# Kernel optimization log

Hardware: AMD Instinct MI355X
Metric: run time of the kernel (lower is better)

## Reference

```python
import jax, jax.numpy as jnp
import numpy as np

# ViT-Small config
L, D, H, HD = 12, 384, 6, 64
P, IMG, NCLS = 16, 224, 1000
NPATCH = (IMG // P) ** 2  # 196
GAMMA, MIN_TOKENS, EPS = 0.5, 16, 1e-6
SCALE = HD ** -0.5


def _ln(x, w, b, eps=1e-6):
    mu = jnp.mean(x, axis=-1, keepdims=True)
    var = jnp.var(x, axis=-1, keepdims=True)
    return (x - mu) * jax.lax.rsqrt(var + eps) * w + b


def _qkv_split(xn, w, b):
    # xn: [B, Nt, D] -> q,k,v each [B, H, Nt, HD]
    B, Nt, _ = xn.shape
    qkv = (xn @ w.T + b).reshape(B, Nt, 3, H, HD).transpose(2, 0, 3, 1, 4)
    return qkv[0], qkv[1], qkv[2]


def _vit_forward(x, patch_w, patch_b, cls_token, pos_embed,
                 ln1_w, ln1_b, qkv_w, qkv_b, proj_w, proj_b,
                 ln2_w, ln2_b, fc1_w, fc1_b, fc2_w, fc2_b,
                 norm_w, norm_b, head_w, head_b, keep_schedule=None):
    B = x.shape[0]
    # patch embed: conv stride 16 -> [B, D, 14, 14] -> [B, 196, D]
    xp = jax.lax.conv_general_dilated(x, patch_w, (P, P), 'VALID',
                                      dimension_numbers=('NCHW', 'OIHW', 'NCHW'))
    xp = xp.reshape(B, D, NPATCH).transpose(0, 2, 1) + patch_b
    cls = jnp.broadcast_to(cls_token, (B, 1, D))
    xt = jnp.concatenate([cls, xp], axis=1) + pos_embed  # [B, 197, D]

    N = NPATCH
    prev_mass = jnp.asarray(1.0, jnp.float32)
    schedule = []
    for l in range(L):
        if keep_schedule is not None:
            keep_idx = keep_schedule[l]
        elif N > MIN_TOKENS:
            # CLS-only attention importance scoring (cheap pass)
            xn = _ln(xt, ln1_w[l], ln1_b[l])
            q, k, v = _qkv_split(xn, qkv_w[l], qkv_b[l])
            a_cls = jax.nn.softmax(jnp.einsum('bhqd,bhkd->bhqk', q[:, :, :1], k) * SCALE, axis=-1)[:, :, 0, :]  # [B,H,Nt]
            vnorm = jnp.linalg.norm(v, axis=-1)  # [B,H,Nt]
            imp = (a_cls * vnorm).mean(axis=1)   # [B,Nt]
            imp_p = imp[:, 1:]                   # patch importance
            mass = jnp.mean(imp_p.sum(-1) / (imp.sum(-1) + EPS))
            keep_ratio = float(jnp.clip(GAMMA * mass / (prev_mass + EPS), 0.0, 1.0))
            N_next = max(MIN_TOKENS, int(N * keep_ratio))
            if N_next < N:
                scores = imp_p.mean(0)  # shared keep set across batch (index_select semantics)
                top = jax.lax.top_k(scores, N_next)[1]
                keep_idx = jnp.concatenate([jnp.zeros((1,), jnp.int32),
                                            jnp.sort(top).astype(jnp.int32) + 1])
            else:
                keep_idx = None
            prev_mass = mass
        else:
            keep_idx = None
        schedule.append(keep_idx)
        if keep_idx is not None:
            xt = jnp.take(xt, keep_idx, axis=1)
            N = int(keep_idx.shape[0]) - 1

        # full transformer block on surviving tokens
        Nt = xt.shape[1]
        xn = _ln(xt, ln1_w[l], ln1_b[l])
        q, k, v = _qkv_split(xn, qkv_w[l], qkv_b[l])
        a = jax.nn.softmax(jnp.einsum('bhqd,bhkd->bhqk', q, k) * SCALE, axis=-1)
        o = jnp.einsum('bhqk,bhkd->bhqd', a, v).transpose(0, 2, 1, 3).reshape(B, Nt, D)
        xt = xt + o @ proj_w[l].T + proj_b[l]
        h = _ln(xt, ln2_w[l], ln2_b[l])
        h = jax.nn.gelu(h @ fc1_w[l].T + fc1_b[l], approximate=False)
        xt = xt + h @ fc2_w[l].T + fc2_b[l]

    xt = _ln(xt, norm_w, norm_b)
    logits = xt[:, 0] @ head_w.T + head_b
    return logits, schedule


def setup_inputs() -> dict:
    key = jax.random.key(0)
    ks = jax.random.split(key, 10)
    rn = lambda k, s, sc=0.02: jax.random.normal(k, s, jnp.float32) * sc
    return {
        'x': jax.random.normal(ks[0], (64, 3, IMG, IMG), jnp.float32),
        'patch_w': rn(ks[1], (D, 3, P, P)),
        'patch_b': jnp.zeros((D,), jnp.float32),
        'cls_token': rn(ks[2], (1, 1, D)),
        'pos_embed': rn(ks[3], (1, NPATCH + 1, D)),
        'ln1_w': jnp.ones((L, D), jnp.float32), 'ln1_b': jnp.zeros((L, D), jnp.float32),
        'qkv_w': rn(ks[4], (L, 3 * D, D)), 'qkv_b': jnp.zeros((L, 3 * D), jnp.float32),
        'proj_w': rn(ks[5], (L, D, D)), 'proj_b': jnp.zeros((L, D), jnp.float32),
        'ln2_w': jnp.ones((L, D), jnp.float32), 'ln2_b': jnp.zeros((L, D), jnp.float32),
        'fc1_w': rn(ks[6], (L, 4 * D, D)), 'fc1_b': jnp.zeros((L, 4 * D), jnp.float32),
        'fc2_w': rn(ks[7], (L, D, 4 * D)), 'fc2_b': jnp.zeros((L, D), jnp.float32),
        'norm_w': jnp.ones((D,), jnp.float32), 'norm_b': jnp.zeros((D,), jnp.float32),
        'head_w': rn(ks[8], (NCLS, D)), 'head_b': jnp.zeros((NCLS,), jnp.float32),
    }


def reference(x, patch_w, patch_b, cls_token, pos_embed, ln1_w, ln1_b, qkv_w, qkv_b,
              proj_w, proj_b, ln2_w, ln2_b, fc1_w, fc1_b, fc2_w, fc2_b,
              norm_w, norm_b, head_w, head_b):
    logits, _ = _vit_forward(x, patch_w, patch_b, cls_token, pos_embed, ln1_w, ln1_b,
                             qkv_w, qkv_b, proj_w, proj_b, ln2_w, ln2_b,
                             fc1_w, fc1_b, fc2_w, fc2_b, norm_w, norm_b, head_w, head_b)
    return logits
```

## Files before the change

kernel.cpp:

```cpp
#include <hip/hip_runtime.h>
#include <hip/hip_bf16.h>

static constexpr int kL = 12;
static constexpr int kD = 384;
static constexpr int kH = 6;
static constexpr int kB = 64;
static constexpr int kNP = 196;
static constexpr int kBAND = 197;
static constexpr int kNCLS = 1000;
static constexpr float kSCALE = 0.125f;
static constexpr float kEPS = 1e-6f;
static constexpr size_t kWQ = (size_t)kB * kH * kBAND * 64;

typedef __attribute__((ext_vector_type(8))) short short8;
typedef __attribute__((ext_vector_type(4))) float f32x4;

__device__ __forceinline__ float gelu_f(float x) {
    return 0.5f * x * (1.0f + erff(x * 0.70710678118654752440f));
}
__device__ __forceinline__ unsigned short f2bf(float x) {
    __hip_bfloat16 h = __float2bfloat16(x);
    return *(unsigned short*)&h;
}
__device__ __forceinline__ float bf2f(unsigned short u) {
    __hip_bfloat16 h = *(__hip_bfloat16*)&u;
    return __bfloat162float(h);
}

__global__ __launch_bounds__(384) void k_init(int* si, float* sf,
                                              const float* __restrict__ cls,
                                              const float* __restrict__ pos,
                                              float* __restrict__ xtA,
                                              float2* __restrict__ pstats) {
    int b = blockIdx.x, c = threadIdx.x;
    float v = cls[c] + pos[c];
    xtA[(size_t)b * kBAND * kD + c] = v;
    __shared__ float r1[384], r2[384];
    r1[c] = v; r2[c] = v * v;
    __syncthreads();
    if (c < 128) { r1[c] += r1[c + 128] + r1[c + 256]; r2[c] += r2[c + 128] + r2[c + 256]; }
    __syncthreads();
    for (int st = 64; st; st >>= 1) {
        if (c < st) { r1[c] += r1[c + st]; r2[c] += r2[c + st]; }
        __syncthreads();
    }
    if (c == 0) {
        pstats[(size_t)(b * kBAND) * 8 + 0] = make_float2(r1[0], r2[0]);
#pragma unroll
        for (int nn = 1; nn < 6; ++nn) pstats[(size_t)(b * kBAND) * 8 + nn] = make_float2(0.f, 0.f);
        if (b == 0) { si[0] = kBAND; sf[0] = 1.0f; }
    }
}

__global__ __launch_bounds__(256) void k_cvtall(
    const float* __restrict__ s0, const float* __restrict__ s1, const float* __restrict__ s2,
    const float* __restrict__ s3, const float* __restrict__ s4,
    __hip_bfloat16* __restrict__ d0, __hip_bfloat16* __restrict__ d1, __hip_bfloat16* __restrict__ d2,
    __hip_bfloat16* __restrict__ d3, __hip_bfloat16* __restrict__ d4) {
    const int c0 = 73728, c1 = 1400832, c2 = 1843200, c3 = 3612672, c4 = 5382144;
    int stride = gridDim.x * 256;
    for (int i = blockIdx.x * 256 + threadIdx.x; i < c4; i += stride) {
        const float* src; __hip_bfloat16* dst; int off;
        if (i < c0)      { src = s0; dst = d0; off = i; }
        else if (i < c1) { src = s1; dst = d1; off = i - c0; }
        else if (i < c2) { src = s2; dst = d2; off = i - c1; }
        else if (i < c3) { src = s3; dst = d3; off = i - c2; }
        else             { src = s4; dst = d4; off = i - c3; }
        float4 v = ((const float4*)src)[off];
        dst[4 * off + 0] = __float2bfloat16(v.x);
        dst[4 * off + 1] = __float2bfloat16(v.y);
        dst[4 * off + 2] = __float2bfloat16(v.z);
        dst[4 * off + 3] = __float2bfloat16(v.w);
    }
}

__global__ __launch_bounds__(256) void k_im2col(const float* __restrict__ x, __hip_bfloat16* __restrict__ A) {
    int pt = blockIdx.x;
    int b = pt / kNP, t = pt - b * kNP;
    int py = t / 14, px = t - py * 14;
    const float* xb = x + (size_t)b * 3 * 224 * 224;
    __hip_bfloat16* arow = A + (size_t)pt * 768;
    for (int k = threadIdx.x; k < 768; k += 256) {
        int c = k >> 8;
        int r = k & 255;
        int ky = r >> 4, kx = r & 15;
        arow[k] = __float2bfloat16(xb[((size_t)c * 224 + py * 16 + ky) * 224 + px * 16 + kx]);
    }
}

template<int OUT_BF16, int ACT_GELU, int MODE, int LNA, int STATS>
__global__ __launch_bounds__(256) void k_mgemm(
    const void* __restrict__ Av, int lda,
    const unsigned short* __restrict__ W, int K,
    const float* __restrict__ bias,
    void* __restrict__ Cv, int ldc,
    const float* __restrict__ R,
    const int* __restrict__ keepR,
    const float* __restrict__ lnw, const float* __restrict__ lnb,
    int rT, int nT, int band,
    const int* __restrict__ NtPtr, int ntConst,
    const float2* __restrict__ pstatsIn, float2* __restrict__ pstatsOut)
{
    __shared__ __align__(16) unsigned char pool[18432];
    unsigned short (*As)[72] = (unsigned short (*)[72])pool;
    unsigned short (*Ws)[72] = (unsigned short (*)[72])(pool + 9216);
    float (*Cs)[66] = (float (*)[66])pool;
    unsigned short (*Cu)[76] = (unsigned short (*)[76])pool;
    __shared__ float mus[64], rss[64];

    int Nt = NtPtr ? NtPtr[0] : ntConst;
    unsigned int rowsTotal = (unsigned int)kB * (unsigned int)Nt;

    int L = blockIdx.x;
    int xcd = L & 7;
    int m = L >> 3;
    int n = m % nT;
    int r = (m / nT) * 8 + xcd;
    if (r >= rT) return;
    unsigned int r0 = (unsigned int)r * 64;
    int n0 = n * 64;
    if (r0 >= rowsTotal) return;

    int tid = threadIdx.x;
    int srow = tid >> 3;
    int scol = (tid & 7) << 3;

    unsigned int rv0 = r0 + srow, rv1 = r0 + srow + 32;
    bool v0 = rv0 < rowsTotal, v1 = rv1 < rowsTotal;
    const unsigned short* ah0 = nullptr; const unsigned short* ah1 = nullptr;
    const float* af0 = nullptr; const float* af1 = nullptr;
    if (v0) {
        unsigned int bb = rv0 / (unsigned int)Nt, tt = rv0 - bb * Nt;
        size_t prow = (size_t)bb * band + tt;
        if (LNA) af0 = (const float*)Av + prow * lda;
        else     ah0 = (const unsigned short*)Av + prow * lda;
    }
    if (v1) {
        unsigned int bb = rv1 / (unsigned int)Nt, tt = rv1 - bb * Nt;
        size_t prow = (size_t)bb * band + tt;
        if (LNA) af1 = (const float*)Av + prow * lda;
        else     ah1 = (const unsigned short*)Av + prow * lda;
    }
    const unsigned short* wp0 = W + (size_t)(n0 + srow) * K;
    const unsigned short* wp1 = W + (size_t)(n0 + srow + 32) * K;

    float mu0 = 0.f, rs0 = 0.f, mu1 = 0.f, rs1 = 0.f;
    if (LNA) {
        if (tid < 64) {
            unsigned int rv = r0 + tid;
            float mu = 0.f, rsd = 0.f;
            if (rv < rowsTotal) {
                unsigned int bb = rv / (unsigned int)Nt, tt = rv - bb * Nt;
                const float2* ps = pstatsIn + ((size_t)bb * band + tt) * 8;
                float s1 = 0.f, s2 = 0.f;
#pragma unroll
                for (int nn = 0; nn < 6; ++nn) { float2 p = ps[nn]; s1 += p.x; s2 += p.y; }
                mu = s1 * (1.f / 384.f);
                float var = fmaxf(s2 * (1.f / 384.f) - mu * mu, 0.f);
                rsd = rsqrtf(var + kEPS);
            }
            mus[tid] = mu; rss[tid] = rsd;
        }
        __syncthreads();
        mu0 = mus[srow]; rs0 = rss[srow];
        mu1 = mus[srow + 32]; rs1 = rss[srow + 32];
    }

    int wave = tid >> 6, lane = tid & 63;
    int wr32 = ((wave >> 1) & 1) * 32, wc32 = (wave & 1) * 32;
    int l15 = lane & 15, l4 = lane >> 4;

    f32x4 acc00 = {}, acc01 = {}, acc10 = {}, acc11 = {};

    for (int k0 = 0; k0 < K; k0 += 64) {
        uint4 zero = make_uint4(0, 0, 0, 0);
        uint4 a0 = zero, a1 = zero;
        uint4 w0 = *(const uint4*)(wp0 + k0 + scol);
        uint4 w1 = *(const uint4*)(wp1 + k0 + scol);
        if (LNA) {
            float4 lw0 = *(const float4*)(lnw + k0 + scol);
            float4 lw1 = *(const float4*)(lnw + k0 + scol + 4);
            float4 lb0 = *(const float4*)(lnb + k0 + scol);
            float4 lb1 = *(const float4*)(lnb + k0 + scol + 4);
            if (v0) {
                float4 x0 = *(const float4*)(af0 + k0 + scol);
                float4 x1 = *(const float4*)(af0 + k0 + scol + 4);
                unsigned short p[8];
                p[0] = f2bf((x0.x - mu0) * rs0 * lw0.x + lb0.x);
                p[1] = f2bf((x0.y - mu0) * rs0 * lw0.y + lb0.y);
                p[2] = f2bf((x0.z - mu0) * rs0 * lw0.z + lb0.z);
                p[3] = f2bf((x0.w - mu0) * rs0 * lw0.w + lb0.w);
                p[4] = f2bf((x1.x - mu0) * rs0 * lw1.x + lb1.x);
                p[5] = f2bf((x1.y - mu0) * rs0 * lw1.y + lb1.y);
                p[6] = f2bf((x1.z - mu0) * rs0 * lw1.z + lb1.z);
                p[7] = f2bf((x1.w - mu0) * rs0 * lw1.w + lb1.w);
                a0 = *(uint4*)p;
            }
            if (v1) {
                float4 x0 = *(const float4*)(af1 + k0 + scol);
                float4 x1 = *(const float4*)(af1 + k0 + scol + 4);
                unsigned short p[8];
                p[0] = f2bf((x0.x - mu1) * rs1 * lw0.x + lb0.x);
                p[1] = f2bf((x0.y - mu1) * rs1 * lw0.y + lb0.y);
                p[2] = f2bf((x0.z - mu1) * rs1 * lw0.z + lb0.z);
                p[3] = f2bf((x0.w - mu1) * rs1 * lw0.w + lb0.w);
                p[4] = f2bf((x1.x - mu1) * rs1 * lw1.x + lb1.x);
                p[5] = f2bf((x1.y - mu1) * rs1 * lw1.y + lb1.y);
                p[6] = f2bf((x1.z - mu1) * rs1 * lw1.z + lb1.z);
                p[7] = f2bf((x1.w - mu1) * rs1 * lw1.w + lb1.w);
                a1 = *(uint4*)p;
            }
        } else {
            a0 = v0 ? *(const uint4*)(ah0 + k0 + scol) : zero;
            a1 = v1 ? *(const uint4*)(ah1 + k0 + scol) : zero;
        }
        __syncthreads();
        *(uint4*)&As[srow][scol] = a0;
        *(uint4*)&As[srow + 32][scol] = a1;
        *(uint4*)&Ws[srow][scol] = w0;
        *(uint4*)&Ws[srow + 32][scol] = w1;
        __syncthreads();
#pragma unroll
        for (int ks = 0; ks < 2; ++ks) {
            short8 af_0 = *(const short8*)&As[wr32 + l15][ks * 32 + l4 * 8];
            short8 af_1 = *(const short8*)&As[wr32 + 16 + l15][ks * 32 + l4 * 8];
            short8 bf_0 = *(const short8*)&Ws[wc32 + l15][ks * 32 + l4 * 8];
            short8 bf_1 = *(const short8*)&Ws[wc32 + 16 + l15][ks * 32 + l4 * 8];
            acc00 = __builtin_amdgcn_mfma_f32_16x16x32_bf16(af_0, bf_0, acc00, 0, 0, 0);
            acc01 = __builtin_amdgcn_mfma_f32_16x16x32_bf16(af_0, bf_1, acc01, 0, 0, 0);
            acc10 = __builtin_amdgcn_mfma_f32_16x16x32_bf16(af_1, bf_0, acc10, 0, 0, 0);
            acc11 = __builtin_amdgcn_mfma_f32_16x16x32_bf16(af_1, bf_1, acc11, 0, 0, 0);
        }
    }

    __syncthreads();
    f32x4 accs[2][2] = { { acc00, acc01 }, { acc10, acc11 } };
#pragma unroll
    for (int fi = 0; fi < 2; ++fi) {
        int lrow = wr32 + fi * 16 + l4 * 4;
        unsigned int rvb = r0 + lrow;
#pragma unroll
        for (int fj = 0; fj < 2; ++fj) {
            int lcol = wc32 + fj * 16 + l15;
            float bv = bias ? bias[n0 + lcol] : 0.f;
#pragma unroll
            for (int rr = 0; rr < 4; ++rr) {
                unsigned int rv = rvb + rr;
                float v = accs[fi][fj][rr] + bv;
                if (ACT_GELU) v = gelu_f(v);
                if (MODE == 2) {
                    if (rv < rowsTotal) {
                        unsigned int bb = rv / (unsigned int)Nt;
                        unsigned int tt = rv - bb * (unsigned int)Nt;
                        v += R[(size_t)(tt + 1) * kD + n0 + lcol];
                    }
                } else if (R && rv < rowsTotal) {
                    unsigned int bb = rv / (unsigned int)Nt;
                    unsigned int tt = rv - bb * (unsigned int)Nt;
                    size_t rrow = keepR ? ((size_t)bb * band + keepR[tt]) : ((size_t)bb * band + tt);
                    v += R[rrow * ldc + n0 + lcol];
                }
                if (OUT_BF16) Cu[lrow + rr][lcol] = f2bf(v);
                else          Cs[lrow + rr][lcol] = v;
            }
        }
    }
    __syncthreads();

    if (OUT_BF16) {
#pragma unroll
        for (int i = 0; i < 2; ++i) {
            int id = tid + (i << 8);
            int row = id >> 3, c2 = id & 7;
            unsigned int rv = r0 + row;
            if (rv < rowsTotal) {
                unsigned int bb = rv / (unsigned int)Nt;
                unsigned int tt = rv - bb * (unsigned int)Nt;
                uint4 val = *(const uint4*)&Cu[row][c2 << 3];
                if (MODE == 1) {
                    int which = n0 >= 768 ? 2 : (n0 >= 384 ? 1 : 0);
                    int hh = (n0 - which * 384) >> 6;
                    *(uint4*)((__hip_bfloat16*)Cv + (size_t)which * kWQ +
                              (((size_t)bb * kH + hh) * kBAND + tt) * 64 + (c2 << 3)) = val;
                } else {
                    size_t prow = (size_t)bb * band + tt;
                    *(uint4*)((__hip_bfloat16*)Cv + prow * ldc + n0 + (c2 << 3)) = val;
                }
            }
        }
    } else {
#pragma unroll
        for (int i = 0; i < 4; ++i) {
            int id = tid + (i << 8);
            int row = id >> 4, c4 = id & 15;
            unsigned int rv = r0 + row;
            if (rv < rowsTotal) {
                unsigned int bb = rv / (unsigned int)Nt;
                unsigned int tt = rv - bb * (unsigned int)Nt;
                float4 val = *(const float4*)&Cs[row][c4 << 2];
                if (MODE == 2) {
                    *(float4*)((float*)Cv + ((size_t)bb * kBAND + tt + 1) * ldc + n0 + (c4 << 2)) = val;
                } else {
                    *(float4*)((float*)Cv + ((size_t)bb * band + tt) * ldc + n0 + (c4 << 2)) = val;
                }
                if (STATS) {
                    float s1 = (val.x + val.y) + (val.z + val.w);
                    float s2 = (val.x * val.x + val.y * val.y) + (val.z * val.z + val.w * val.w);
#pragma unroll
                    for (int off = 1; off < 16; off <<= 1) {
                        s1 += __shfl_xor(s1, off, 64);
                        s2 += __shfl_xor(s2, off, 64);
                    }
                    if (c4 == 0) {
                        size_t sridx = (MODE == 2) ? ((size_t)bb * kBAND + tt + 1)
                                                   : ((size_t)bb * band + tt);
                        pstatsOut[sridx * 8 + n] = make_float2(s1, s2);
                    }
                }
            }
        }
    }
}

__global__ __launch_bounds__(256) void k_decA(const __hip_bfloat16* __restrict__ qsplit,
                                              float* __restrict__ imph, float* __restrict__ sabh,
                                              const int* __restrict__ si) {
    int Nt = si[0];
    if (Nt - 1 <= 16) return;
    int tid = threadIdx.x, w = tid >> 6, lane = tid & 63;
    int bh = blockIdx.x;
    __shared__ float qs[64];
    __shared__ float sdot[224], svn[224];
    __shared__ float red[256];
    const __hip_bfloat16* qp = qsplit + (size_t)bh * kBAND * 64;
    const __hip_bfloat16* kp = qsplit + kWQ + (size_t)bh * kBAND * 64;
    const __hip_bfloat16* vp = qsplit + 2 * kWQ + (size_t)bh * kBAND * 64;
    if (tid < 64) qs[tid] = __bfloat162float(qp[tid]);
    __syncthreads();
    float qv = qs[lane];
    for (int j = w; j < Nt; j += 8) {
        int j2 = j + 4;
        bool has2 = j2 < Nt;
        float k1 = __bfloat162float(kp[(size_t)j * 64 + lane]);
        float v1 = __bfloat162float(vp[(size_t)j * 64 + lane]);
        float k2 = has2 ? __bfloat162float(kp[(size_t)j2 * 64 + lane]) : 0.f;
        float v2 = has2 ? __bfloat162float(vp[(size_t)j2 * 64 + lane]) : 0.f;
        float p1 = qv * k1, n1 = v1 * v1;
        float p2 = qv * k2, n2 = v2 * v2;
#pragma unroll
        for (int off = 1; off < 64; off <<= 1) {
            p1 += __shfl_xor(p1, off, 64); n1 += __shfl_xor(n1, off, 64);
            p2 += __shfl_xor(p2, off, 64); n2 += __shfl_xor(n2, off, 64);
        }
        if (lane == 0) {
            sdot[j] = p1 * kSCALE; svn[j] = sqrtf(n1);
            if (has2) { sdot[j2] = p2 * kSCALE; svn[j2] = sqrtf(n2); }
        }
    }
    __syncthreads();
    float s = (tid < Nt) ? sdot[tid] : -INFINITY;
    red[tid] = s; __syncthreads();
    for (int st = 128; st; st >>= 1) { if (tid < st) red[tid] = fmaxf(red[tid], red[tid + st]); __syncthreads(); }
    float mmax = red[0]; __syncthreads();
    float e = (tid < Nt) ? expf(s - mmax) : 0.f;
    red[tid] = e; __syncthreads();
    for (int st = 128; st; st >>= 1) { if (tid < st) red[tid] += red[tid + st]; __syncthreads(); }
    float inv = 1.f / red[0];
    float val = (tid < Nt) ? e * inv * svn[tid] : 0.f;
    if (tid < Nt) imph[(size_t)bh * kBAND + tid] = val;
    __syncthreads();
    red[tid] = val; __syncthreads();
    for (int st = 128; st; st >>= 1) { if (tid < st) red[tid] += red[tid + st]; __syncthreads(); }
    if (tid == 0) { sabh[2 * bh] = red[0]; sabh[2 * bh + 1] = val; }
}

__global__ __launch_bounds__(256) void k_decB(int* __restrict__ si, float* __restrict__ sf,
                                              const float* __restrict__ imph,
                                              const float* __restrict__ sabh,
                                              int* __restrict__ keep) {
    int Nt = si[0];
    int tid = threadIdx.x;
    if (Nt - 1 <= 16) {
        for (int j = tid; j < Nt; j += 256) keep[j] = j;
        return;
    }
    int N = Nt - 1;
    __shared__ float red[256];
    float v = 0.f;
    if (tid < kB) {
        float sa = 0.f, i0 = 0.f;
#pragma unroll
        for (int hh = 0; hh < kH; ++hh) {
            sa += sabh[2 * (tid * kH + hh)];
            i0 += sabh[2 * (tid * kH + hh) + 1];
        }
        sa *= (1.f / 6.f); i0 *= (1.f / 6.f);
        v = (sa - i0) / (sa + kEPS);
    }
    red[tid] = v; __syncthreads();
    for (int st = 128; st; st >>= 1) { if (tid < st) red[tid] += red[tid + st]; __syncthreads(); }
    float mass = red[0] * (1.f / 64.f);
    float prev = sf[0];
    float ratio = 0.5f * mass / (prev + kEPS);
    ratio = fminf(fmaxf(ratio, 0.f), 1.f);
    int N_next = (int)((double)N * (double)ratio);
    if (N_next < 16) N_next = 16;
    if (tid == 0) sf[0] = mass;
    __syncthreads();
    if (N_next >= N) {
        for (int j = tid; j < Nt; j += 256) keep[j] = j;
        return;
    }
    __shared__ float sc[200];
    __shared__ int flag[200];
    if (tid < N) {
        float a0 = 0.f, a1 = 0.f, a2 = 0.f, a3 = 0.f;
        const float* p = imph + tid + 1;
#pragma unroll 4
        for (int q = 0; q < kB * kH; q += 4) {
            a0 += p[(size_t)(q + 0) * kBAND];
            a1 += p[(size_t)(q + 1) * kBAND];
            a2 += p[(size_t)(q + 2) * kBAND];
            a3 += p[(size_t)(q + 3) * kBAND];
        }
        sc[tid] = (a0 + a1) + (a2 + a3);
    }
    __syncthreads();
    if (tid < N) {
        float s2 = sc[tid];
        int rank = 0;
        for (int i = 0; i < N; ++i) {
            float o2 = sc[i];
            rank += (o2 > s2) || (o2 == s2 && i < tid);
        }
        flag[tid] = (rank < N_next) ? 1 : 0;
    }
    __syncthreads();
    if (tid == 0) {
        keep[0] = 0;
        int pos = 1;
        for (int j = 0; j < N; ++j) if (flag[j]) keep[pos++] = j + 1;
        si[0] = N_next + 1;
    }
}

__global__ __launch_bounds__(256) void k_attn2(const __hip_bfloat16* __restrict__ qsplit,
                                               __hip_bfloat16* __restrict__ o,
                                               const int* __restrict__ si,
                                               const int* __restrict__ keep) {
    __shared__ __align__(16) unsigned short Kb[224][72];
    __shared__ __align__(16) unsigned short Vt[64][228];
    __shared__ __align__(16) unsigned short Pb[4][16][228];
    int Nt = si[0];
    int bh = blockIdx.x;
    int b = bh / kH, h = bh - b * kH;
    int tid = threadIdx.x, w = tid >> 6, lane = tid & 63;
    int l15 = lane & 15, l4 = lane >> 4;
    int nJT = (Nt + 15) >> 4;
    int nKT = (Nt + 31) >> 5;
    int NTP = nKT << 5;

    const unsigned short* qb = (const unsigned short*)qsplit + (size_t)bh * kBAND * 64;
    const unsigned short* kb = (const unsigned short*)qsplit + kWQ + (size_t)bh * kBAND * 64;
    const unsigned short* vb = (const unsigned short*)qsplit + 2 * kWQ + (size_t)bh * kBAND * 64;

    {
        int rr = tid >> 3;
        int c8 = (tid & 7) << 3;
        for (int r = rr; r < NTP; r += 32) {
            uint4 kv = make_uint4(0, 0, 0, 0), vv = make_uint4(0, 0, 0, 0);
            if (r < Nt) {
                int old = keep[r];
                kv = *(const uint4*)(kb + ((size_t)old << 6) + c8);
                vv = *(const uint4*)(vb + ((size_t)old << 6) + c8);
            }
            *(uint4*)&Kb[r][c8] = kv;
            const unsigned short* vs = (const unsigned short*)&vv;
#pragma unroll
            for (int e = 0; e < 8; ++e) Vt[c8 + e][r] = vs[e];
        }
    }
    __syncthreads();

    for (int strip = w; strip < nJT; strip += 4) {
        int tq = (strip << 4) + l15;
        int told = (tq < Nt) ? keep[tq] : 0;
        const unsigned short* qrow = qb + ((size_t)told << 6) + (l4 << 3);
        short8 qf0 = *(const short8*)(qrow);
        short8 qf1 = *(const short8*)(qrow + 32);

        f32x4 sv[13];
#pragma unroll
        for (int jt = 0; jt < 13; ++jt) {
            if (jt < nJT) {
                const unsigned short* kr = &Kb[(jt << 4) + l15][l4 << 3];
                short8 kf0 = *(const short8*)(kr);
                short8 kf1 = *(const short8*)(kr + 32);
                f32x4 a = {};
                a = __builtin_amdgcn_mfma_f32_16x16x32_bf16(qf0, kf0, a, 0, 0, 0);
                a = __builtin_amdgcn_mfma_f32_16x16x32_bf16(qf1, kf1, a, 0, 0, 0);
                sv[jt] = a;
            }
        }
        float mx[4] = { -INFINITY, -INFINITY, -INFINITY, -INFINITY };
#pragma unroll
        for (int jt = 0; jt < 13; ++jt) if (jt < nJT) {
            bool ok = ((jt << 4) + l15) < Nt;
#pragma unroll
            for (int r = 0; r < 4; ++r) {
                float s = ok ? sv[jt][r] * kSCALE : -INFINITY;
                sv[jt][r] = s;
                mx[r] = fmaxf(mx[r], s);
            }
        }
#pragma unroll
        for (int r = 0; r < 4; ++r) {
            mx[r] = fmaxf(mx[r], __shfl_xor(mx[r], 1, 64));
            mx[r] = fmaxf(mx[r], __shfl_xor(mx[r], 2, 64));
            mx[r] = fmaxf(mx[r], __shfl_xor(mx[r], 4, 64));
            mx[r] = fmaxf(mx[r], __shfl_xor(mx[r], 8, 64));
        }
        float sm[4] = { 0.f, 0.f, 0.f, 0.f };
#pragma unroll
        for (int jt = 0; jt < 13; ++jt) if (jt < nJT) {
#pragma unroll
            for (int r = 0; r < 4; ++r) {
                float p = expf(sv[jt][r] - mx[r]);
                sv[jt][r] = p;
                sm[r] += p;
            }
        }
#pragma unroll
        for (int r = 0; r < 4; ++r) {
            sm[r] += __shfl_xor(sm[r], 1, 64);
            sm[r] += __shfl_xor(sm[r], 2, 64);
            sm[r] += __shfl_xor(sm[r], 4, 64);
            sm[r] += __shfl_xor(sm[r], 8, 64);
            sm[r] = 1.f / sm[r];
        }
#pragma unroll
        for (int jt = 0; jt < 13; ++jt) if (jt < nJT) {
#pragma unroll
            for (int r = 0; r < 4; ++r)
                Pb[w][(l4 << 2) + r][(jt << 4) + l15] = f2bf(sv[jt][r] * sm[r]);
        }
        for (int c = (nJT << 4) + lane; c < NTP; c += 64) {
#pragma unroll
            for (int rr2 = 0; rr2 < 16; ++rr2) Pb[w][rr2][c] = 0;
        }
        asm volatile("s_waitcnt lgkmcnt(0)" ::: "memory");
        __builtin_amdgcn_sched_barrier(0);

        f32x4 oacc[4] = { {}, {}, {}, {} };
#pragma unroll
        for (int kt = 0; kt < 7; ++kt) if (kt < nKT) {
            short8 pf = *(const short8*)&Pb[w][l15][(kt << 5) + (l4 << 3)];
#pragma unroll
            for (int dt = 0; dt < 4; ++dt) {
                short8 vf = *(const short8*)&Vt[(dt << 4) + l15][(kt << 5) + (l4 << 3)];
                oacc[dt] = __builtin_amdgcn_mfma_f32_16x16x32_bf16(pf, vf, oacc[dt], 0, 0, 0);
            }
        }
#pragma unroll
        for (int dt = 0; dt < 4; ++dt) {
#pragma unroll
            for (int r = 0; r < 4; ++r) {
                int tqo = (strip << 4) + (l4 << 2) + r;
                if (tqo < Nt)
                    o[((size_t)b * kBAND + tqo) * kD + h * 64 + (dt << 4) + l15] =
                        __float2bfloat16(oacc[dt][r]);
            }
        }
    }
}

__global__ __launch_bounds__(256) void k_head(const float* __restrict__ X,
                                              const float* __restrict__ nw, const float* __restrict__ nb,
                                              const float* __restrict__ hw, const float* __restrict__ hb,
                                              float* __restrict__ out) {
    int b = blockIdx.x >> 2;
    int tid = threadIdx.x;
    __shared__ float xs[384];
    __shared__ float red[256];
    const float* row = X + (size_t)b * kBAND * kD;
    float s1 = 0.f, s2 = 0.f;
    for (int c = tid; c < 384; c += 256) { float v = row[c]; xs[c] = v; s1 += v; s2 += v * v; }
    red[tid] = s1; __syncthreads();
    for (int st = 128; st; st >>= 1) { if (tid < st) red[tid] += red[tid + st]; __syncthreads(); }
    float sum = red[0]; __syncthreads();
    red[tid] = s2; __syncthreads();
    for (int st = 128; st; st >>= 1) { if (tid < st) red[tid] += red[tid + st]; __syncthreads(); }
    float sq = red[0];
    float mu = sum * (1.f / 384.f);
    float var = fmaxf(sq * (1.f / 384.f) - mu * mu, 0.f);
    float rs = rsqrtf(var + kEPS);
    __syncthreads();
    for (int c = tid; c < 384; c += 256) xs[c] = (xs[c] - mu) * rs * nw[c] + nb[c];
    __syncthreads();
    int n = ((blockIdx.x & 3) << 8) + tid;
    if (n >= kNCLS) return;
    const float* wrow = hw + (size_t)n * kD;
    float acc = 0.f;
#pragma unroll 8
    for (int d = 0; d < kD; d += 4) {
        float4 w4 = *(const float4*)(wrow + d);
        acc += xs[d] * w4.x + xs[d + 1] * w4.y + xs[d + 2] * w4.z + xs[d + 3] * w4.w;
    }
    out[(size_t)b * kNCLS + n] = acc + hb[n];
}

extern "C" void kernel_launch(void* const* d_in, const int* in_sizes, int n_in,
                              void* d_out, int out_size, void* d_ws, size_t ws_size,
                              hipStream_t stream) {
    const float* x       = (const float*)d_in[0];
    const float* patch_w = (const float*)d_in[1];
    const float* patch_b = (const float*)d_in[2];
    const float* cls_tok = (const float*)d_in[3];
    const float* pos     = (const float*)d_in[4];
    const float* ln1w    = (const float*)d_in[5];
    const float* ln1b    = (const float*)d_in[6];
    const float* qkvw    = (const float*)d_in[7];
    const float* qkvb    = (const float*)d_in[8];
    const float* projw   = (const float*)d_in[9];
    const float* projb   = (const float*)d_in[10];
    const float* ln2w    = (const float*)d_in[11];
    const float* ln2b    = (const float*)d_in[12];
    const float* fc1w    = (const float*)d_in[13];
    const float* fc1b    = (const float*)d_in[14];
    const float* fc2w    = (const float*)d_in[15];
    const float* fc2b    = (const float*)d_in[16];
    const float* normw   = (const float*)d_in[17];
    const float* normb   = (const float*)d_in[18];
    const float* headw   = (const float*)d_in[19];
    const float* headb   = (const float*)d_in[20];
    float* out = (float*)d_out;

    char* ws = (char*)d_ws;
    const size_t MB = 1024ull * 1024ull;
    int*   si   = (int*)ws;
    float* sf   = (float*)(ws + 64);
    int*   keep = (int*)(ws + 256);
    float* sabh = (float*)(ws + 4096);
    float* imph = (float*)(ws + 16384);
    float* xtA  = (float*)(ws + 1 * MB);
    float* xtB  = (float*)(ws + 21 * MB);
    __hip_bfloat16* obuf = (__hip_bfloat16*)(ws + 41 * MB);
    __hip_bfloat16* Aim    = (__hip_bfloat16*)(ws + 51 * MB);
    __hip_bfloat16* qsplit = (__hip_bfloat16*)(ws + 51 * MB);
    __hip_bfloat16* hbuf   = (__hip_bfloat16*)(ws + 51 * MB);
    __hip_bfloat16* wpat = (__hip_bfloat16*)(ws + 110 * MB);
    __hip_bfloat16* wqkv = (__hip_bfloat16*)(ws + 111 * MB);
    __hip_bfloat16* wprj = (__hip_bfloat16*)(ws + 122 * MB);
    __hip_bfloat16* wfc1 = (__hip_bfloat16*)(ws + 126 * MB);
    __hip_bfloat16* wfc2 = (__hip_bfloat16*)(ws + 141 * MB);
    float2* pstats = (float2*)(ws + 156 * MB);

    k_init<<<64, 384, 0, stream>>>(si, sf, cls_tok, pos, xtA, pstats);
    k_cvtall<<<2048, 256, 0, stream>>>(patch_w, qkvw, projw, fc1w, fc2w,
                                       wpat, wqkv, wprj, wfc1, wfc2);

    k_im2col<<<kB * kNP, 256, 0, stream>>>(x, Aim);
    k_mgemm<0, 0, 2, 0, 1><<<8 * 6 * 25, 256, 0, stream>>>(
        (const void*)Aim, 768, (const unsigned short*)wpat, 768,
        patch_b, xtA, kD, pos, (const int*)nullptr,
        (const float*)nullptr, (const float*)nullptr,
        196, 6, 196, (const int*)nullptr, 196,
        (const float2*)nullptr, pstats);

    float* cur = xtA; float* oth = xtB;
    for (int l = 0; l < kL; ++l) {
        const float* l1w = ln1w + l * kD;  const float* l1b = ln1b + l * kD;
        const __hip_bfloat16* qw = wqkv + (size_t)l * 1152 * kD;
        const float* qb = qkvb + l * 1152;
        const __hip_bfloat16* pw = wprj + (size_t)l * kD * kD;
        const float* pb = projb + l * kD;
        const float* l2w = ln2w + l * kD;  const float* l2b = ln2b + l * kD;
        const __hip_bfloat16* f1w = wfc1 + (size_t)l * 1536 * kD;
        const float* f1b = fc1b + l * 1536;
        const __hip_bfloat16* f2w = wfc2 + (size_t)l * kD * 1536;
        const float* f2b = fc2b + l * kD;

        k_mgemm<1, 0, 1, 1, 0><<<8 * 18 * 25, 256, 0, stream>>>(
            (const void*)cur, kD, (const unsigned short*)qw, kD,
            qb, qsplit, 1152, (const float*)nullptr, (const int*)nullptr,
            l1w, l1b, 197, 18, kBAND, si, 0,
            (const float2*)pstats, (float2*)nullptr);
        k_decA<<<kB * kH, 256, 0, stream>>>(qsplit, imph, sabh, si);
        k_decB<<<1, 256, 0, stream>>>(si, sf, imph, sabh, keep);
        k_attn2<<<kB * kH, 256, 0, stream>>>(qsplit, obuf, si, keep);
        k_mgemm<0, 0, 0, 0, 1><<<8 * 6 * 25, 256, 0, stream>>>(
            (const void*)obuf, kD, (const unsigned short*)pw, kD,
            pb, oth, kD, cur, keep,
            (const float*)nullptr, (const float*)nullptr,
            197, 6, kBAND, si, 0,
            (const float2*)nullptr, pstats);
        { float* tmp = cur; cur = oth; oth = tmp; }
        k_mgemm<1, 1, 0, 1, 0><<<8 * 24 * 25, 256, 0, stream>>>(
            (const void*)cur, kD, (const unsigned short*)f1w, kD,
            f1b, hbuf, 1536, (const float*)nullptr, (const int*)nullptr,
            l2w, l2b, 197, 24, kBAND, si, 0,
            (const float2*)pstats, (float2*)nullptr);
        k_mgemm<0, 0, 0, 0, 1><<<8 * 6 * 25, 256, 0, stream>>>(
            (const void*)hbuf, 1536, (const unsigned short*)f2w, 1536,
            f2b, cur, kD, cur, (const int*)nullptr,
            (const float*)nullptr, (const float*)nullptr,
            197, 6, kBAND, si, 0,
            (const float2*)nullptr, pstats);
    }

    k_head<<<kB * 4, 256, 0, stream>>>(cur, normw, normb, headw, headb, out);
}
```

Before: 1.251 ms.

## Enlarge GEMM tiles to 128x128 and transpose importance buffer for coalesced reduction

The MFMA GEMM kernel moves from 64x64 to 128x128 output tiles, with each wave computing a 4x4 grid of 16x16 fragments. The epilogue is staged in two halves through enlarged shared memory, and all launch grids are resized to match. Separately, the per-head importance array is stored token-major so the single-block keep-selection kernel can reduce it with coalesced float4 loads split across four segments. The larger tiles raise data reuse per block but use more registers and shared memory, and they give fewer blocks, which may lower occupancy and wave count as the token count shrinks.

```diff
diff --git a/kernel.cpp b/kernel.cpp
--- a/kernel.cpp
+++ b/kernel.cpp
@@ -11,6 +11,7 @@
 static constexpr float kSCALE = 0.125f;
 static constexpr float kEPS = 1e-6f;
 static constexpr size_t kWQ = (size_t)kB * kH * kBAND * 64;
+static constexpr int kBH = kB * kH;
 
 typedef __attribute__((ext_vector_type(8))) short short8;
 typedef __attribute__((ext_vector_type(4))) float f32x4;
@@ -21,10 +22,6 @@
 __device__ __forceinline__ unsigned short f2bf(float x) {
     __hip_bfloat16 h = __float2bfloat16(x);
     return *(unsigned short*)&h;
-}
-__device__ __forceinline__ float bf2f(unsigned short u) {
-    __hip_bfloat16 h = *(__hip_bfloat16*)&u;
-    return __bfloat162float(h);
 }
 
 __global__ __launch_bounds__(384) void k_init(int* si, float* sf,
@@ -101,12 +98,12 @@
     const int* __restrict__ NtPtr, int ntConst,
     const float2* __restrict__ pstatsIn, float2* __restrict__ pstatsOut)
 {
-    __shared__ __align__(16) unsigned char pool[18432];
+    __shared__ __align__(16) unsigned char pool[36928];
     unsigned short (*As)[72] = (unsigned short (*)[72])pool;
-    unsigned short (*Ws)[72] = (unsigned short (*)[72])(pool + 9216);
-    float (*Cs)[66] = (float (*)[66])pool;
-    unsigned short (*Cu)[76] = (unsigned short (*)[76])pool;
-    __shared__ float mus[64], rss[64];
+    unsigned short (*Ws)[72] = (unsigned short (*)[72])(pool + 18432);
+    float (*Cs)[136] = (float (*)[136])pool;
+    unsigned short (*Cu)[136] = (unsigned short (*)[136])pool;
+    __shared__ float mus[128], rss[128];
 
     int Nt = NtPtr ? NtPtr[0] : ntConst;
     unsigned int rowsTotal = (unsigned int)kB * (unsigned int)Nt;
@@ -117,208 +114,201 @@
     int n = m % nT;
     int r = (m / nT) * 8 + xcd;
     if (r >= rT) return;
-    unsigned int r0 = (unsigned int)r * 64;
-    int n0 = n * 64;
+    unsigned int r0 = (unsigned int)r * 128;
+    int n0 = n * 128;
     if (r0 >= rowsTotal) return;
 
     int tid = threadIdx.x;
-    int srow = tid >> 3;
-    int scol = (tid & 7) << 3;
-
-    unsigned int rv0 = r0 + srow, rv1 = r0 + srow + 32;
-    bool v0 = rv0 < rowsTotal, v1 = rv1 < rowsTotal;
-    const unsigned short* ah0 = nullptr; const unsigned short* ah1 = nullptr;
-    const float* af0 = nullptr; const float* af1 = nullptr;
-    if (v0) {
-        unsigned int bb = rv0 / (unsigned int)Nt, tt = rv0 - bb * Nt;
+    int srow = tid >> 1;
+    int scol = (tid & 1) << 5;
+
+    unsigned int rvs = r0 + srow;
+    bool vA = rvs < rowsTotal;
+    const unsigned short* ah = nullptr; const float* af = nullptr;
+    if (vA) {
+        unsigned int bb = rvs / (unsigned int)Nt, tt = rvs - bb * Nt;
         size_t prow = (size_t)bb * band + tt;
-        if (LNA) af0 = (const float*)Av + prow * lda;
-        else     ah0 = (const unsigned short*)Av + prow * lda;
-    }
-    if (v1) {
-        unsigned int bb = rv1 / (unsigned int)Nt, tt = rv1 - bb * Nt;
-        size_t prow = (size_t)bb * band + tt;
-        if (LNA) af1 = (const float*)Av + prow * lda;
-        else     ah1 = (const unsigned short*)Av + prow * lda;
-    }
-    const unsigned short* wp0 = W + (size_t)(n0 + srow) * K;
-    const unsigned short* wp1 = W + (size_t)(n0 + srow + 32) * K;
-
-    float mu0 = 0.f, rs0 = 0.f, mu1 = 0.f, rs1 = 0.f;
+        if (LNA) af = (const float*)Av + prow * lda;
+        else     ah = (const unsigned short*)Av + prow * lda;
+    }
+    const unsigned short* wp = W + (size_t)(n0 + srow) * K;
+
+    float mu = 0.f, rsd = 0.f;
     if (LNA) {
-        if (tid < 64) {
+        if (tid < 128) {
             unsigned int rv = r0 + tid;
-            float mu = 0.f, rsd = 0.f;
+            float m_ = 0.f, rr_ = 0.f;
             if (rv < rowsTotal) {
                 unsigned int bb = rv / (unsigned int)Nt, tt = rv - bb * Nt;
                 const float2* ps = pstatsIn + ((size_t)bb * band + tt) * 8;
                 float s1 = 0.f, s2 = 0.f;
 #pragma unroll
                 for (int nn = 0; nn < 6; ++nn) { float2 p = ps[nn]; s1 += p.x; s2 += p.y; }
-                mu = s1 * (1.f / 384.f);
-                float var = fmaxf(s2 * (1.f / 384.f) - mu * mu, 0.f);
-                rsd = rsqrtf(var + kEPS);
-            }
-            mus[tid] = mu; rss[tid] = rsd;
+                m_ = s1 * (1.f / 384.f);
+                float var = fmaxf(s2 * (1.f / 384.f) - m_ * m_, 0.f);
+                rr_ = rsqrtf(var + kEPS);
+            }
+            mus[tid] = m_; rss[tid] = rr_;
         }
         __syncthreads();
-        mu0 = mus[srow]; rs0 = rss[srow];
-        mu1 = mus[srow + 32]; rs1 = rss[srow + 32];
+        mu = mus[srow]; rsd = rss[srow];
     }
 
     int wave = tid >> 6, lane = tid & 63;
-    int wr32 = ((wave >> 1) & 1) * 32, wc32 = (wave & 1) * 32;
+    int wr = (wave >> 1) << 6;
+    int wc = (wave & 1) << 6;
     int l15 = lane & 15, l4 = lane >> 4;
 
-    f32x4 acc00 = {}, acc01 = {}, acc10 = {}, acc11 = {};
+    f32x4 acc[4][4];
+#pragma unroll
+    for (int i = 0; i < 4; ++i)
+#pragma unroll
+        for (int j = 0; j < 4; ++j) acc[i][j] = (f32x4){};
 
     for (int k0 = 0; k0 < K; k0 += 64) {
-        uint4 zero = make_uint4(0, 0, 0, 0);
-        uint4 a0 = zero, a1 = zero;
-        uint4 w0 = *(const uint4*)(wp0 + k0 + scol);
-        uint4 w1 = *(const uint4*)(wp1 + k0 + scol);
-        if (LNA) {
-            float4 lw0 = *(const float4*)(lnw + k0 + scol);
-            float4 lw1 = *(const float4*)(lnw + k0 + scol + 4);
-            float4 lb0 = *(const float4*)(lnb + k0 + scol);
-            float4 lb1 = *(const float4*)(lnb + k0 + scol + 4);
-            if (v0) {
-                float4 x0 = *(const float4*)(af0 + k0 + scol);
-                float4 x1 = *(const float4*)(af0 + k0 + scol + 4);
-                unsigned short p[8];
-                p[0] = f2bf((x0.x - mu0) * rs0 * lw0.x + lb0.x);
-                p[1] = f2bf((x0.y - mu0) * rs0 * lw0.y + lb0.y);
-                p[2] = f2bf((x0.z - mu0) * rs0 * lw0.z + lb0.z);
-                p[3] = f2bf((x0.w - mu0) * rs0 * lw0.w + lb0.w);
-                p[4] = f2bf((x1.x - mu0) * rs0 * lw1.x + lb1.x);
-                p[5] = f2bf((x1.y - mu0) * rs0 * lw1.y + lb1.y);
-                p[6] = f2bf((x1.z - mu0) * rs0 * lw1.z + lb1.z);
-                p[7] = f2bf((x1.w - mu0) * rs0 * lw1.w + lb1.w);
-                a0 = *(uint4*)p;
-            }
-            if (v1) {
-                float4 x0 = *(const float4*)(af1 + k0 + scol);
-                float4 x1 = *(const float4*)(af1 + k0 + scol + 4);
-                unsigned short p[8];
-                p[0] = f2bf((x0.x - mu1) * rs1 * lw0.x + lb0.x);
-                p[1] = f2bf((x0.y - mu1) * rs1 * lw0.y + lb0.y);
-                p[2] = f2bf((x0.z - mu1) * rs1 * lw0.z + lb0.z);
-                p[3] = f2bf((x0.w - mu1) * rs1 * lw0.w + lb0.w);
-                p[4] = f2bf((x1.x - mu1) * rs1 * lw1.x + lb1.x);
-                p[5] = f2bf((x1.y - mu1) * rs1 * lw1.y + lb1.y);
-                p[6] = f2bf((x1.z - mu1) * rs1 * lw1.z + lb1.z);
-                p[7] = f2bf((x1.w - mu1) * rs1 * lw1.w + lb1.w);
-                a1 = *(uint4*)p;
-            }
-        } else {
-            a0 = v0 ? *(const uint4*)(ah0 + k0 + scol) : zero;
-            a1 = v1 ? *(const uint4*)(ah1 + k0 + scol) : zero;
+        uint4 a[4], wv[4];
+#pragma unroll
+        for (int e = 0; e < 4; ++e) {
+            wv[e] = *(const uint4*)(wp + k0 + scol + (e << 3));
+            if (LNA) {
+                if (vA) {
+                    const float* ap = af + k0 + scol + (e << 3);
+                    float4 x0 = *(const float4*)(ap);
+                    float4 x1 = *(const float4*)(ap + 4);
+                    float4 lw0 = *(const float4*)(lnw + k0 + scol + (e << 3));
+                    float4 lw1 = *(const float4*)(lnw + k0 + scol + (e << 3) + 4);
+                    float4 lb0 = *(const float4*)(lnb + k0 + scol + (e << 3));
+                    float4 lb1 = *(const float4*)(lnb + k0 + scol + (e << 3) + 4);
+                    unsigned short p[8];
+                    p[0] = f2bf((x0.x - mu) * rsd * lw0.x + lb0.x);
+                    p[1] = f2bf((x0.y - mu) * rsd * lw0.y + lb0.y);
+                    p[2] = f2bf((x0.z - mu) * rsd * lw0.z + lb0.z);
+                    p[3] = f2bf((x0.w - mu) * rsd * lw0.w + lb0.w);
+                    p[4] = f2bf((x1.x - mu) * rsd * lw1.x + lb1.x);
+                    p[5] = f2bf((x1.y - mu) * rsd * lw1.y + lb1.y);
+                    p[6] = f2bf((x1.z - mu) * rsd * lw1.z + lb1.z);
+                    p[7] = f2bf((x1.w - mu) * rsd * lw1.w + lb1.w);
+                    a[e] = *(uint4*)p;
+                } else a[e] = make_uint4(0, 0, 0, 0);
+            } else {
+                a[e] = vA ? *(const uint4*)(ah + k0 + scol + (e << 3)) : make_uint4(0, 0, 0, 0);
+            }
         }
         __syncthreads();
-        *(uint4*)&As[srow][scol] = a0;
-        *(uint4*)&As[srow + 32][scol] = a1;
-        *(uint4*)&Ws[srow][scol] = w0;
-        *(uint4*)&Ws[srow + 32][scol] = w1;
+#pragma unroll
+        for (int e = 0; e < 4; ++e) {
+            *(uint4*)&As[srow][scol + (e << 3)] = a[e];
+            *(uint4*)&Ws[srow][scol + (e << 3)] = wv[e];
+        }
         __syncthreads();
 #pragma unroll
         for (int ks = 0; ks < 2; ++ks) {
-            short8 af_0 = *(const short8*)&As[wr32 + l15][ks * 32 + l4 * 8];
-            short8 af_1 = *(const short8*)&As[wr32 + 16 + l15][ks * 32 + l4 * 8];
-            short8 bf_0 = *(const short8*)&Ws[wc32 + l15][ks * 32 + l4 * 8];
-            short8 bf_1 = *(const short8*)&Ws[wc32 + 16 + l15][ks * 32 + l4 * 8];
-            acc00 = __builtin_amdgcn_mfma_f32_16x16x32_bf16(af_0, bf_0, acc00, 0, 0, 0);
-            acc01 = __builtin_amdgcn_mfma_f32_16x16x32_bf16(af_0, bf_1, acc01, 0, 0, 0);
-            acc10 = __builtin_amdgcn_mfma_f32_16x16x32_bf16(af_1, bf_0, acc10, 0, 0, 0);
-            acc11 = __builtin_amdgcn_mfma_f32_16x16x32_bf16(af_1, bf_1, acc11, 0, 0, 0);
-        }
-    }
-
-    __syncthreads();
-    f32x4 accs[2][2] = { { acc00, acc01 }, { acc10, acc11 } };
-#pragma unroll
-    for (int fi = 0; fi < 2; ++fi) {
-        int lrow = wr32 + fi * 16 + l4 * 4;
-        unsigned int rvb = r0 + lrow;
-#pragma unroll
-        for (int fj = 0; fj < 2; ++fj) {
-            int lcol = wc32 + fj * 16 + l15;
-            float bv = bias ? bias[n0 + lcol] : 0.f;
-#pragma unroll
-            for (int rr = 0; rr < 4; ++rr) {
-                unsigned int rv = rvb + rr;
-                float v = accs[fi][fj][rr] + bv;
-                if (ACT_GELU) v = gelu_f(v);
-                if (MODE == 2) {
-                    if (rv < rowsTotal) {
-                        unsigned int bb = rv / (unsigned int)Nt;
-                        unsigned int tt = rv - bb * (unsigned int)Nt;
-                        v += R[(size_t)(tt + 1) * kD + n0 + lcol];
+            short8 afr[4], bfr[4];
+#pragma unroll
+            for (int i = 0; i < 4; ++i)
+                afr[i] = *(const short8*)&As[wr + (i << 4) + l15][(ks << 5) + (l4 << 3)];
+#pragma unroll
+            for (int j = 0; j < 4; ++j)
+                bfr[j] = *(const short8*)&Ws[wc + (j << 4) + l15][(ks << 5) + (l4 << 3)];
+#pragma unroll
+            for (int i = 0; i < 4; ++i)
+#pragma unroll
+                for (int j = 0; j < 4; ++j)
+                    acc[i][j] = __builtin_amdgcn_mfma_f32_16x16x32_bf16(afr[i], bfr[j], acc[i][j], 0, 0, 0);
+        }
+    }
+
+    __syncthreads();
+#pragma unroll
+    for (int half = 0; half < 2; ++half) {
+        if ((wave >> 1) == half) {
+#pragma unroll
+            for (int i = 0; i < 4; ++i) {
+                int lrow = (i << 4) + (l4 << 2);
+                unsigned int rvb = r0 + (half << 6) + lrow;
+#pragma unroll
+                for (int j = 0; j < 4; ++j) {
+                    int lcol = wc + (j << 4) + l15;
+                    float bv = bias ? bias[n0 + lcol] : 0.f;
+#pragma unroll
+                    for (int rr = 0; rr < 4; ++rr) {
+                        unsigned int rv = rvb + rr;
+                        float v = acc[i][j][rr] + bv;
+                        if (ACT_GELU) v = gelu_f(v);
+                        if (MODE == 2) {
+                            if (rv < rowsTotal) {
+                                unsigned int bb = rv / (unsigned int)Nt;
+                                unsigned int tt = rv - bb * (unsigned int)Nt;
+                                v += R[(size_t)(tt + 1) * kD + n0 + lcol];
+                            }
+                        } else if (R && rv < rowsTotal) {
+                            unsigned int bb = rv / (unsigned int)Nt;
+                            unsigned int tt = rv - bb * (unsigned int)Nt;
+                            size_t rrow = keepR ? ((size_t)bb * band + keepR[tt]) : ((size_t)bb * band + tt);
+                            v += R[rrow * ldc + n0 + lcol];
+                        }
+                        if (OUT_BF16) Cu[lrow + rr][lcol] = f2bf(v);
+                        else          Cs[lrow + rr][lcol] = v;
                     }
-                } else if (R && rv < rowsTotal) {
+                }
+            }
+        }
+        __syncthreads();
+        if (OUT_BF16) {
+#pragma unroll
+            for (int i2 = 0; i2 < 4; ++i2) {
+                int id = tid + (i2 << 8);
+                int row = id >> 4, c2 = id & 15;
+                unsigned int rv = r0 + (half << 6) + row;
+                if (rv < rowsTotal) {
                     unsigned int bb = rv / (unsigned int)Nt;
                     unsigned int tt = rv - bb * (unsigned int)Nt;
-                    size_t rrow = keepR ? ((size_t)bb * band + keepR[tt]) : ((size_t)bb * band + tt);
-                    v += R[rrow * ldc + n0 + lcol];
-                }
-                if (OUT_BF16) Cu[lrow + rr][lcol] = f2bf(v);
-                else          Cs[lrow + rr][lcol] = v;
-            }
-        }
-    }
-    __syncthreads();
-
-    if (OUT_BF16) {
-#pragma unroll
-        for (int i = 0; i < 2; ++i) {
-            int id = tid + (i << 8);
-            int row = id >> 3, c2 = id & 7;
-            unsigned int rv = r0 + row;
-            if (rv < rowsTotal) {
-                unsigned int bb = rv / (unsigned int)Nt;
-                unsigned int tt = rv - bb * (unsigned int)Nt;
-                uint4 val = *(const uint4*)&Cu[row][c2 << 3];
-                if (MODE == 1) {
-                    int which = n0 >= 768 ? 2 : (n0 >= 384 ? 1 : 0);
-                    int hh = (n0 - which * 384) >> 6;
-                    *(uint4*)((__hip_bfloat16*)Cv + (size_t)which * kWQ +
-                              (((size_t)bb * kH + hh) * kBAND + tt) * 64 + (c2 << 3)) = val;
-                } else {
-                    size_t prow = (size_t)bb * band + tt;
-                    *(uint4*)((__hip_bfloat16*)Cv + prow * ldc + n0 + (c2 << 3)) = val;
-                }
-            }
-        }
-    } else {
-#pragma unroll
-        for (int i = 0; i < 4; ++i) {
-            int id = tid + (i << 8);
-            int row = id >> 4, c4 = id & 15;
-            unsigned int rv = r0 + row;
-            if (rv < rowsTotal) {
-                unsigned int bb = rv / (unsigned int)Nt;
-                unsigned int tt = rv - bb * (unsigned int)Nt;
-                float4 val = *(const float4*)&Cs[row][c4 << 2];
-                if (MODE == 2) {
-                    *(float4*)((float*)Cv + ((size_t)bb * kBAND + tt + 1) * ldc + n0 + (c4 << 2)) = val;
-                } else {
-                    *(float4*)((float*)Cv + ((size_t)bb * band + tt) * ldc + n0 + (c4 << 2)) = val;
-                }
-                if (STATS) {
-                    float s1 = (val.x + val.y) + (val.z + val.w);
-                    float s2 = (val.x * val.x + val.y * val.y) + (val.z * val.z + val.w * val.w);
-#pragma unroll
-                    for (int off = 1; off < 16; off <<= 1) {
-                        s1 += __shfl_xor(s1, off, 64);
-                        s2 += __shfl_xor(s2, off, 64);
-                    }
-                    if (c4 == 0) {
-                        size_t sridx = (MODE == 2) ? ((size_t)bb * kBAND + tt + 1)
-                                                   : ((size_t)bb * band + tt);
-                        pstatsOut[sridx * 8 + n] = make_float2(s1, s2);
+                    uint4 val = *(const uint4*)&Cu[row][c2 << 3];
+                    if (MODE == 1) {
+                        int gc = n0 + (c2 << 3);
+                        int which = gc >= 768 ? 2 : (gc >= 384 ? 1 : 0);
+                        int hh = (gc - which * 384) >> 6;
+                        *(uint4*)((__hip_bfloat16*)Cv + (size_t)which * kWQ +
+                                  (((size_t)bb * kH + hh) * kBAND + tt) * 64 + (gc & 63)) = val;
+                    } else {
+                        size_t prow = (size_t)bb * band + tt;
+                        *(uint4*)((__hip_bfloat16*)Cv + prow * ldc + n0 + (c2 << 3)) = val;
                     }
                 }
             }
-        }
+        } else {
+#pragma unroll
+            for (int i2 = 0; i2 < 8; ++i2) {
+                int id = tid + (i2 << 8);
+                int row = id >> 5, c4 = id & 31;
+                unsigned int rv = r0 + (half << 6) + row;
+                if (rv < rowsTotal) {
+                    unsigned int bb = rv / (unsigned int)Nt;
+                    unsigned int tt = rv - bb * (unsigned int)Nt;
+                    float4 val = *(const float4*)&Cs[row][c4 << 2];
+                    if (MODE == 2) {
+                        *(float4*)((float*)Cv + ((size_t)bb * kBAND + tt + 1) * ldc + n0 + (c4 << 2)) = val;
+                    } else {
+                        *(float4*)((float*)Cv + ((size_t)bb * band + tt) * ldc + n0 + (c4 << 2)) = val;
+                    }
+                    if (STATS) {
+                        float s1 = (val.x + val.y) + (val.z + val.w);
+                        float s2 = (val.x * val.x + val.y * val.y) + (val.z * val.z + val.w * val.w);
+#pragma unroll
+                        for (int off = 1; off < 16; off <<= 1) {
+                            s1 += __shfl_xor(s1, off, 64);
+                            s2 += __shfl_xor(s2, off, 64);
+                        }
+                        if ((c4 & 15) == 0) {
+                            size_t sridx = (MODE == 2) ? ((size_t)bb * kBAND + tt + 1)
+                                                       : ((size_t)bb * band + tt);
+                            pstatsOut[sridx * 8 + (n << 1) + (c4 >> 4)] = make_float2(s1, s2);
+                        }
+                    }
+                }
+            }
+        }
+        __syncthreads();
     }
 }
 
@@ -367,7 +357,7 @@
     for (int st = 128; st; st >>= 1) { if (tid < st) red[tid] += red[tid + st]; __syncthreads(); }
     float inv = 1.f / red[0];
     float val = (tid < Nt) ? e * inv * svn[tid] : 0.f;
-    if (tid < Nt) imph[(size_t)bh * kBAND + tid] = val;
+    if (tid < Nt) imph[(size_t)tid * kBH + bh] = val;
     __syncthreads();
     red[tid] = val; __syncthreads();
     for (int st = 128; st; st >>= 1) { if (tid < st) red[tid] += red[tid + st]; __syncthreads(); }
@@ -411,20 +401,25 @@
         for (int j = tid; j < Nt; j += 256) keep[j] = j;
         return;
     }
+    __shared__ float scq[200][4];
     __shared__ float sc[200];
     __shared__ int flag[200];
-    if (tid < N) {
+    for (int task = tid; task < N * 4; task += 256) {
+        int row = task >> 2, seg = task & 3;
+        const float4* p = (const float4*)(imph + (size_t)(row + 1) * kBH) + seg * 24;
         float a0 = 0.f, a1 = 0.f, a2 = 0.f, a3 = 0.f;
-        const float* p = imph + tid + 1;
-#pragma unroll 4
-        for (int q = 0; q < kB * kH; q += 4) {
-            a0 += p[(size_t)(q + 0) * kBAND];
-            a1 += p[(size_t)(q + 1) * kBAND];
-            a2 += p[(size_t)(q + 2) * kBAND];
-            a3 += p[(size_t)(q + 3) * kBAND];
-        }
-        sc[tid] = (a0 + a1) + (a2 + a3);
-    }
+#pragma unroll
+        for (int q = 0; q < 24; q += 4) {
+            float4 x0 = p[q + 0], x1 = p[q + 1], x2 = p[q + 2], x3 = p[q + 3];
+            a0 += (x0.x + x0.y) + (x0.z + x0.w);
+            a1 += (x1.x + x1.y) + (x1.z + x1.w);
+            a2 += (x2.x + x2.y) + (x2.z + x2.w);
+            a3 += (x3.x + x3.y) + (x3.z + x3.w);
+        }
+        scq[row][seg] = (a0 + a1) + (a2 + a3);
+    }
+    __syncthreads();
+    if (tid < N) sc[tid] = (scq[tid][0] + scq[tid][1]) + (scq[tid][2] + scq[tid][3]);
     __syncthreads();
     if (tid < N) {
         float s2 = sc[tid];
@@ -660,11 +655,11 @@
                                        wpat, wqkv, wprj, wfc1, wfc2);
 
     k_im2col<<<kB * kNP, 256, 0, stream>>>(x, Aim);
-    k_mgemm<0, 0, 2, 0, 1><<<8 * 6 * 25, 256, 0, stream>>>(
+    k_mgemm<0, 0, 2, 0, 1><<<8 * 3 * 13, 256, 0, stream>>>(
         (const void*)Aim, 768, (const unsigned short*)wpat, 768,
         patch_b, xtA, kD, pos, (const int*)nullptr,
         (const float*)nullptr, (const float*)nullptr,
-        196, 6, 196, (const int*)nullptr, 196,
+        98, 3, 196, (const int*)nullptr, 196,
         (const float2*)nullptr, pstats);
 
     float* cur = xtA; float* oth = xtB;
@@ -680,31 +675,31 @@
         const __hip_bfloat16* f2w = wfc2 + (size_t)l * kD * 1536;
         const float* f2b = fc2b + l * kD;
 
-        k_mgemm<1, 0, 1, 1, 0><<<8 * 18 * 25, 256, 0, stream>>>(
+        k_mgemm<1, 0, 1, 1, 0><<<8 * 9 * 13, 256, 0, stream>>>(
             (const void*)cur, kD, (const unsigned short*)qw, kD,
             qb, qsplit, 1152, (const float*)nullptr, (const int*)nullptr,
-            l1w, l1b, 197, 18, kBAND, si, 0,
+            l1w, l1b, 99, 9, kBAND, si, 0,
             (const float2*)pstats, (float2*)nullptr);
         k_decA<<<kB * kH, 256, 0, stream>>>(qsplit, imph, sabh, si);
         k_decB<<<1, 256, 0, stream>>>(si, sf, imph, sabh, keep);
         k_attn2<<<kB * kH, 256, 0, stream>>>(qsplit, obuf, si, keep);
-        k_mgemm<0, 0, 0, 0, 1><<<8 * 6 * 25, 256, 0, stream>>>(
+        k_mgemm<0, 0, 0, 0, 1><<<8 * 3 * 13, 256, 0, stream>>>(
             (const void*)obuf, kD, (const unsigned short*)pw, kD,
             pb, oth, kD, cur, keep,
             (const float*)nullptr, (const float*)nullptr,
-            197, 6, kBAND, si, 0,
+            99, 3, kBAND, si, 0,
             (const float2*)nullptr, pstats);
         { float* tmp = cur; cur = oth; oth = tmp; }
-        k_mgemm<1, 1, 0, 1, 0><<<8 * 24 * 25, 256, 0, stream>>>(
+        k_mgemm<1, 1, 0, 1, 0><<<8 * 12 * 13, 256, 0, stream>>>(
             (const void*)cur, kD, (const unsigned short*)f1w, kD,
             f1b, hbuf, 1536, (const float*)nullptr, (const int*)nullptr,
-            l2w, l2b, 197, 24, kBAND, si, 0,
+            l2w, l2b, 99, 12, kBAND, si, 0,
             (const float2*)pstats, (float2*)nullptr);
-        k_mgemm<0, 0, 0, 0, 1><<<8 * 6 * 25, 256, 0, stream>>>(
+        k_mgemm<0, 0, 0, 0, 1><<<8 * 3 * 13, 256, 0, stream>>>(
             (const void*)hbuf, 1536, (const unsigned short*)f2w, 1536,
             f2b, cur, kD, cur, (const int*)nullptr,
             (const float*)nullptr, (const float*)nullptr,
-            197, 6, kBAND, si, 0,
+            99, 3, kBAND, si, 0,
             (const float2*)nullptr, pstats);
     }
 
```

Measured after the change: 3.356 ms. +168.3%, slower.
